# Kernel optimization log

Hardware: AMD Instinct MI355X
Metric: run time of the kernel (lower is better)

The kernel has to match this reference:

```python
import jax, jax.numpy as jnp
import numpy as np

N = 4_194_304  # number of sample points


def _make_C():
    # Faithful reproduction of the module's compliance matrix (including the
    # asymmetry: Ci[2,0]=Ci[2,1]=-vp, NOT -vp/Ep, exactly as in the source).
    vp, Ep = 0.4, 0.21
    Ci = np.zeros((6, 6), dtype=np.float64)
    Ci[0, 0] = 1 / Ep;  Ci[0, 1] = -vp / Ep; Ci[0, 2] = -vp / Ep
    Ci[1, 0] = -vp / Ep; Ci[1, 1] = 1 / Ep;  Ci[1, 2] = -vp / Ep
    Ci[2, 0] = -vp;      Ci[2, 1] = -vp;     Ci[2, 2] = 1 / Ep
    Ci[3, 3] = 2 * (1 + vp) / Ep
    Ci[4, 4] = 2 * (1 + vp) / Ep
    Ci[5, 5] = 2 * (1 + vp) / Ep
    return jnp.asarray(np.linalg.inv(Ci), dtype=jnp.float32)

_C = _make_C()  # [6, 6] stiffness matrix


def setup_inputs() -> dict:
    key = jax.random.key(0)
    k1, k2, k3, k4 = jax.random.split(key, 4)
    return {
        "grad_u": jax.random.normal(k1, (N, 3), dtype=jnp.float32),
        "grad_v": jax.random.normal(k2, (N, 3), dtype=jnp.float32),
        "grad_w": jax.random.normal(k3, (N, 3), dtype=jnp.float32),
        "gt_sdf": jax.random.normal(k4, (N,), dtype=jnp.float32),
    }


def reference(grad_u, grad_v, grad_w, gt_sdf):
    # Build per-point strain tensor in Voigt-like notation: [N, 6]
    et = jnp.stack([
        grad_u[:, 0],
        grad_v[:, 1],
        grad_w[:, 2],
        (grad_u[:, 1] + grad_v[:, 0]) * 0.5,
        (grad_u[:, 2] + grad_w[:, 0]) * 0.5,
        (grad_w[:, 1] + grad_v[:, 2]) * 0.5,
    ], axis=1)
    # Per-point quadratic form et_i^T C et_i == diag(et @ C @ et.T) without the
    # O(N^2) intermediate the torch code materializes.
    q = jnp.einsum('ni,ij,nj->n', et, _C, et)
    # Mask = points with gt_sdf < 1e-8 (index_select in torch; masked here so
    # shapes stay static under jit). Excluded points contribute 0 to the norm.
    mask = gt_sdf < 1e-8
    qm = jnp.where(mask, q, 0.0)
    count = jnp.sum(mask).astype(et.dtype)  # et.shape[0] after index_select
    W = jnp.sqrt(jnp.sum(qm * qm))           # L2 norm of the diagonal vector
    return W / count
```

## Files before the change

### kernel.cpp

```cpp
#include <hip/hip_runtime.h>
#include <math.h>

struct CParams {
    float b[3][3];
    float s;
};

static CParams make_C() {
    const double vp = 0.4, Ep = 0.21;
    double A[3][3] = {
        {1.0 / Ep, -vp / Ep, -vp / Ep},
        {-vp / Ep, 1.0 / Ep, -vp / Ep},
        {-vp,      -vp,      1.0 / Ep},
    };
    double inv[3][3] = {{1, 0, 0}, {0, 1, 0}, {0, 0, 1}};
    for (int col = 0; col < 3; ++col) {
        int piv = col;
        for (int r = col + 1; r < 3; ++r)
            if (fabs(A[r][col]) > fabs(A[piv][col])) piv = r;
        if (piv != col) {
            for (int c = 0; c < 3; ++c) {
                double t = A[col][c]; A[col][c] = A[piv][c]; A[piv][c] = t;
                t = inv[col][c]; inv[col][c] = inv[piv][c]; inv[piv][c] = t;
            }
        }
        double d = A[col][col];
        for (int c = 0; c < 3; ++c) { A[col][c] /= d; inv[col][c] /= d; }
        for (int r = 0; r < 3; ++r) {
            if (r == col) continue;
            double f = A[r][col];
            for (int c = 0; c < 3; ++c) {
                A[r][c] -= f * A[col][c];
                inv[r][c] -= f * inv[col][c];
            }
        }
    }
    CParams p;
    for (int i = 0; i < 3; ++i)
        for (int j = 0; j < 3; ++j)
            p.b[i][j] = (float)inv[i][j];
    p.s = (float)(Ep / (2.0 * (1.0 + vp)));
    return p;
}

static const CParams g_C = make_C();

#define MAXB 2048
#define TPB  256
#define TILE 256
#define F4A  192

#define ZERO4 make_float4(0.0f, 0.0f, 0.0f, 0.0f)

__global__ __launch_bounds__(TPB) void biomech_reduce(
    const float* __restrict__ gu, const float* __restrict__ gv,
    const float* __restrict__ gw, const float* __restrict__ gs,
    float* __restrict__ ws, int n, CParams C)
{
    __shared__ float4 buf[TPB / 64][3][F4A];

    const int wave    = threadIdx.x >> 6;
    const int lane    = threadIdx.x & 63;
    const int nwaves  = gridDim.x * (TPB / 64);
    const int ngroups = n / TILE;

    const float4* u4 = (const float4*)gu;
    const float4* v4 = (const float4*)gv;
    const float4* w4 = (const float4*)gw;

    float sumq2 = 0.0f, cnt = 0.0f;

    float4 pu0 = ZERO4, pu1 = ZERO4, pu2 = ZERO4;
    float4 pv0 = ZERO4, pv1 = ZERO4, pv2 = ZERO4;
    float4 pw0 = ZERO4, pw1 = ZERO4, pw2 = ZERO4;
    float  ps0 = 1.0f, ps1 = 1.0f, ps2 = 1.0f, ps3 = 1.0f;

    {
        const int g = blockIdx.x * (TPB / 64) + wave;
        if (g < ngroups) {
            const int b  = g * F4A;
            const int sb = g * TILE;
            pu0 = u4[b + lane]; pu1 = u4[b + 64 + lane]; pu2 = u4[b + 128 + lane];
            pv0 = v4[b + lane]; pv1 = v4[b + 64 + lane]; pv2 = v4[b + 128 + lane];
            pw0 = w4[b + lane]; pw1 = w4[b + 64 + lane]; pw2 = w4[b + 128 + lane];
            ps0 = gs[sb + lane];       ps1 = gs[sb + 64 + lane];
            ps2 = gs[sb + 128 + lane]; ps3 = gs[sb + 192 + lane];
        }
    }

    for (int gb = blockIdx.x * (TPB / 64); gb < ngroups; gb += nwaves) {
        const int g  = gb + wave;
        const int gn = g + nwaves;

        float4 nu0 = ZERO4, nu1 = ZERO4, nu2 = ZERO4;
        float4 nv0 = ZERO4, nv1 = ZERO4, nv2 = ZERO4;
        float4 nw0 = ZERO4, nw1 = ZERO4, nw2 = ZERO4;
        float  ns0 = 1.0f, ns1 = 1.0f, ns2 = 1.0f, ns3 = 1.0f;
        if (gn < ngroups) {
            const int b  = gn * F4A;
            const int sb = gn * TILE;
            nu0 = u4[b + lane]; nu1 = u4[b + 64 + lane]; nu2 = u4[b + 128 + lane];
            nv0 = v4[b + lane]; nv1 = v4[b + 64 + lane]; nv2 = v4[b + 128 + lane];
            nw0 = w4[b + lane]; nw1 = w4[b + 64 + lane]; nw2 = w4[b + 128 + lane];
            ns0 = gs[sb + lane];       ns1 = gs[sb + 64 + lane];
            ns2 = gs[sb + 128 + lane]; ns3 = gs[sb + 192 + lane];
        }

        if (g < ngroups) {
            buf[wave][0][lane] = pu0; buf[wave][0][64 + lane] = pu1; buf[wave][0][128 + lane] = pu2;
            buf[wave][1][lane] = pv0; buf[wave][1][64 + lane] = pv1; buf[wave][1][128 + lane] = pv2;
            buf[wave][2][lane] = pw0; buf[wave][2][64 + lane] = pw1; buf[wave][2][128 + lane] = pw2;
        }

        __syncthreads();

        if (g < ngroups) {
            const float* bu = (const float*)&buf[wave][0][0];
            const float* bv = (const float*)&buf[wave][1][0];
            const float* bw = (const float*)&buf[wave][2][0];
            const float sd[4] = {ps0, ps1, ps2, ps3};

#pragma unroll
            for (int k = 0; k < 4; ++k) {
                const int p = lane + (k << 6);
                float u0 = bu[3 * p], u1 = bu[3 * p + 1], u2 = bu[3 * p + 2];
                float v0 = bv[3 * p], v1 = bv[3 * p + 1], v2 = bv[3 * p + 2];
                float w0 = bw[3 * p], w1 = bw[3 * p + 1], w2 = bw[3 * p + 2];

                float e0 = u0, e1 = v1, e2 = w2;
                float e3 = 0.5f * (u1 + v0);
                float e4 = 0.5f * (u2 + w0);
                float e5 = 0.5f * (w1 + v2);

                float q = e0 * (C.b[0][0] * e0 + C.b[0][1] * e1 + C.b[0][2] * e2)
                        + e1 * (C.b[1][0] * e0 + C.b[1][1] * e1 + C.b[1][2] * e2)
                        + e2 * (C.b[2][0] * e0 + C.b[2][1] * e1 + C.b[2][2] * e2)
                        + C.s * (e3 * e3 + e4 * e4 + e5 * e5);

                bool m = sd[k] < 1e-8f;
                float qm = m ? q : 0.0f;
                sumq2 += qm * qm;
                cnt   += m ? 1.0f : 0.0f;
            }
        }

        __syncthreads();

        pu0 = nu0; pu1 = nu1; pu2 = nu2;
        pv0 = nv0; pv1 = nv1; pv2 = nv2;
        pw0 = nw0; pw1 = nw1; pw2 = nw2;
        ps0 = ns0; ps1 = ns1; ps2 = ns2; ps3 = ns3;
    }

    if (blockIdx.x == 0 && threadIdx.x == 0) {
        for (int i = (n / TILE) * TILE; i < n; ++i) {
            float e0 = gu[3 * i + 0];
            float e1 = gv[3 * i + 1];
            float e2 = gw[3 * i + 2];
            float e3 = 0.5f * (gu[3 * i + 1] + gv[3 * i + 0]);
            float e4 = 0.5f * (gu[3 * i + 2] + gw[3 * i + 0]);
            float e5 = 0.5f * (gw[3 * i + 1] + gv[3 * i + 2]);
            float q = e0 * (C.b[0][0] * e0 + C.b[0][1] * e1 + C.b[0][2] * e2)
                    + e1 * (C.b[1][0] * e0 + C.b[1][1] * e1 + C.b[1][2] * e2)
                    + e2 * (C.b[2][0] * e0 + C.b[2][1] * e1 + C.b[2][2] * e2)
                    + C.s * (e3 * e3 + e4 * e4 + e5 * e5);
            bool m = gs[i] < 1e-8f;
            float qm = m ? q : 0.0f;
            sumq2 += qm * qm;
            cnt   += m ? 1.0f : 0.0f;
        }
    }

#pragma unroll
    for (int off = 32; off > 0; off >>= 1) {
        sumq2 += __shfl_down(sumq2, off);
        cnt   += __shfl_down(cnt, off);
    }

    __shared__ float ssum[4], scnt[4];
    if (lane == 0) { ssum[wave] = sumq2; scnt[wave] = cnt; }
    __syncthreads();
    if (threadIdx.x == 0) {
        float s2 = 0.0f, c2 = 0.0f;
#pragma unroll
        for (int i = 0; i < 4; ++i) { s2 += ssum[i]; c2 += scnt[i]; }
        ws[blockIdx.x]        = s2;
        ws[MAXB + blockIdx.x] = c2;
    }
}

__global__ __launch_bounds__(256) void biomech_finalize(
    const float* __restrict__ ws, float* __restrict__ out, int nb)
{
    float s = 0.0f, c = 0.0f;
    for (int i = threadIdx.x; i < nb; i += 256) {
        s += ws[i];
        c += ws[MAXB + i];
    }
#pragma unroll
    for (int off = 32; off > 0; off >>= 1) {
        s += __shfl_down(s, off);
        c += __shfl_down(c, off);
    }
    __shared__ float ssum[4], scnt[4];
    const int wave = threadIdx.x >> 6;
    const int lane = threadIdx.x & 63;
    if (lane == 0) { ssum[wave] = s; scnt[wave] = c; }
    __syncthreads();
    if (threadIdx.x == 0) {
        float s2 = ssum[0] + ssum[1] + ssum[2] + ssum[3];
        float c2 = scnt[0] + scnt[1] + scnt[2] + scnt[3];
        out[0] = sqrtf(s2) / c2;
    }
}

extern "C" void kernel_launch(void* const* d_in, const int* in_sizes, int n_in,
                              void* d_out, int out_size, void* d_ws, size_t ws_size,
                              hipStream_t stream) {
    const float* gu = (const float*)d_in[0];
    const float* gv = (const float*)d_in[1];
    const float* gw = (const float*)d_in[2];
    const float* gs = (const float*)d_in[3];
    float* ws = (float*)d_ws;
    float* out = (float*)d_out;

    const int n = in_sizes[3];
    const int ngroups = n / TILE;
    const int wpb = TPB / 64;

    int grid = (ngroups + wpb - 1) / wpb;
    if (grid > 1024) grid = 1024;
    if (grid > MAXB) grid = MAXB;
    while (grid > 1 && (size_t)(MAXB + grid) * sizeof(float) > ws_size) grid >>= 1;
    if (grid < 1) grid = 1;

    biomech_reduce<<<grid, TPB, 0, stream>>>(gu, gv, gw, gs, ws, n, g_C);
    biomech_finalize<<<1, 256, 0, stream>>>(ws, out, grid);
}
```

Measured before the change: 179.3 us.

## Replace LDS-staged transpose with per-thread 4-point float4 loads

Removes the shared-memory staging buffer, the software prefetch and the two block barriers per iteration. Each thread now loads three consecutive float4s per gradient array plus one float4 of sdf, covering four points, and unpacks them in registers. The grid cap also rises from 1024 to 2048 blocks. Global loads become strided per lane (each lane reads 48 contiguous bytes), which may coalesce less well than the previous lane-contiguous pattern, in exchange for no LDS traffic and no synchronisation.

```diff
diff --git a/kernel.cpp b/kernel.cpp
--- a/kernel.cpp
+++ b/kernel.cpp
@@ -47,127 +47,68 @@
 
 #define MAXB 2048
 #define TPB  256
-#define TILE 256
-#define F4A  192
 
-#define ZERO4 make_float4(0.0f, 0.0f, 0.0f, 0.0f)
+__device__ __forceinline__ void accum_point(
+    float u0, float u1, float u2,
+    float v0, float v1, float v2,
+    float w0, float w1, float w2,
+    float sd, const CParams& C, float& sumq2, float& cnt)
+{
+    float e0 = u0, e1 = v1, e2 = w2;
+    float e3 = 0.5f * (u1 + v0);
+    float e4 = 0.5f * (u2 + w0);
+    float e5 = 0.5f * (w1 + v2);
+
+    float q = e0 * (C.b[0][0] * e0 + C.b[0][1] * e1 + C.b[0][2] * e2)
+            + e1 * (C.b[1][0] * e0 + C.b[1][1] * e1 + C.b[1][2] * e2)
+            + e2 * (C.b[2][0] * e0 + C.b[2][1] * e1 + C.b[2][2] * e2)
+            + C.s * (e3 * e3 + e4 * e4 + e5 * e5);
+
+    bool m = sd < 1e-8f;
+    float qm = m ? q : 0.0f;
+    sumq2 += qm * qm;
+    cnt   += m ? 1.0f : 0.0f;
+}
 
 __global__ __launch_bounds__(TPB) void biomech_reduce(
     const float* __restrict__ gu, const float* __restrict__ gv,
     const float* __restrict__ gw, const float* __restrict__ gs,
     float* __restrict__ ws, int n, CParams C)
 {
-    __shared__ float4 buf[TPB / 64][3][F4A];
-
-    const int wave    = threadIdx.x >> 6;
-    const int lane    = threadIdx.x & 63;
-    const int nwaves  = gridDim.x * (TPB / 64);
-    const int ngroups = n / TILE;
+    const int tid    = blockIdx.x * TPB + threadIdx.x;
+    const int stride = gridDim.x * TPB;
+    const int nvec   = n >> 2;
 
     const float4* u4 = (const float4*)gu;
     const float4* v4 = (const float4*)gv;
     const float4* w4 = (const float4*)gw;
+    const float4* s4 = (const float4*)gs;
 
     float sumq2 = 0.0f, cnt = 0.0f;
 
-    float4 pu0 = ZERO4, pu1 = ZERO4, pu2 = ZERO4;
-    float4 pv0 = ZERO4, pv1 = ZERO4, pv2 = ZERO4;
-    float4 pw0 = ZERO4, pw1 = ZERO4, pw2 = ZERO4;
-    float  ps0 = 1.0f, ps1 = 1.0f, ps2 = 1.0f, ps3 = 1.0f;
+    for (int i = tid; i < nvec; i += stride) {
+        const int b = 3 * i;
+        float4 a0 = u4[b], a1 = u4[b + 1], a2 = u4[b + 2];
+        float4 b0 = v4[b], b1 = v4[b + 1], b2 = v4[b + 2];
+        float4 c0 = w4[b], c1 = w4[b + 1], c2 = w4[b + 2];
+        float4 sd = s4[i];
 
-    {
-        const int g = blockIdx.x * (TPB / 64) + wave;
-        if (g < ngroups) {
-            const int b  = g * F4A;
-            const int sb = g * TILE;
-            pu0 = u4[b + lane]; pu1 = u4[b + 64 + lane]; pu2 = u4[b + 128 + lane];
-            pv0 = v4[b + lane]; pv1 = v4[b + 64 + lane]; pv2 = v4[b + 128 + lane];
-            pw0 = w4[b + lane]; pw1 = w4[b + 64 + lane]; pw2 = w4[b + 128 + lane];
-            ps0 = gs[sb + lane];       ps1 = gs[sb + 64 + lane];
-            ps2 = gs[sb + 128 + lane]; ps3 = gs[sb + 192 + lane];
-        }
-    }
-
-    for (int gb = blockIdx.x * (TPB / 64); gb < ngroups; gb += nwaves) {
-        const int g  = gb + wave;
-        const int gn = g + nwaves;
-
-        float4 nu0 = ZERO4, nu1 = ZERO4, nu2 = ZERO4;
-        float4 nv0 = ZERO4, nv1 = ZERO4, nv2 = ZERO4;
-        float4 nw0 = ZERO4, nw1 = ZERO4, nw2 = ZERO4;
-        float  ns0 = 1.0f, ns1 = 1.0f, ns2 = 1.0f, ns3 = 1.0f;
-        if (gn < ngroups) {
-            const int b  = gn * F4A;
-            const int sb = gn * TILE;
-            nu0 = u4[b + lane]; nu1 = u4[b + 64 + lane]; nu2 = u4[b + 128 + lane];
-            nv0 = v4[b + lane]; nv1 = v4[b + 64 + lane]; nv2 = v4[b + 128 + lane];
-            nw0 = w4[b + lane]; nw1 = w4[b + 64 + lane]; nw2 = w4[b + 128 + lane];
-            ns0 = gs[sb + lane];       ns1 = gs[sb + 64 + lane];
-            ns2 = gs[sb + 128 + lane]; ns3 = gs[sb + 192 + lane];
-        }
-
-        if (g < ngroups) {
-            buf[wave][0][lane] = pu0; buf[wave][0][64 + lane] = pu1; buf[wave][0][128 + lane] = pu2;
-            buf[wave][1][lane] = pv0; buf[wave][1][64 + lane] = pv1; buf[wave][1][128 + lane] = pv2;
-            buf[wave][2][lane] = pw0; buf[wave][2][64 + lane] = pw1; buf[wave][2][128 + lane] = pw2;
-        }
-
-        __syncthreads();
-
-        if (g < ngroups) {
-            const float* bu = (const float*)&buf[wave][0][0];
-            const float* bv = (const float*)&buf[wave][1][0];
-            const float* bw = (const float*)&buf[wave][2][0];
-            const float sd[4] = {ps0, ps1, ps2, ps3};
-
-#pragma unroll
-            for (int k = 0; k < 4; ++k) {
-                const int p = lane + (k << 6);
-                float u0 = bu[3 * p], u1 = bu[3 * p + 1], u2 = bu[3 * p + 2];
-                float v0 = bv[3 * p], v1 = bv[3 * p + 1], v2 = bv[3 * p + 2];
-                float w0 = bw[3 * p], w1 = bw[3 * p + 1], w2 = bw[3 * p + 2];
-
-                float e0 = u0, e1 = v1, e2 = w2;
-                float e3 = 0.5f * (u1 + v0);
-                float e4 = 0.5f * (u2 + w0);
-                float e5 = 0.5f * (w1 + v2);
-
-                float q = e0 * (C.b[0][0] * e0 + C.b[0][1] * e1 + C.b[0][2] * e2)
-                        + e1 * (C.b[1][0] * e0 + C.b[1][1] * e1 + C.b[1][2] * e2)
-                        + e2 * (C.b[2][0] * e0 + C.b[2][1] * e1 + C.b[2][2] * e2)
-                        + C.s * (e3 * e3 + e4 * e4 + e5 * e5);
-
-                bool m = sd[k] < 1e-8f;
-                float qm = m ? q : 0.0f;
-                sumq2 += qm * qm;
-                cnt   += m ? 1.0f : 0.0f;
-            }
-        }
-
-        __syncthreads();
-
-        pu0 = nu0; pu1 = nu1; pu2 = nu2;
-        pv0 = nv0; pv1 = nv1; pv2 = nv2;
-        pw0 = nw0; pw1 = nw1; pw2 = nw2;
-        ps0 = ns0; ps1 = ns1; ps2 = ns2; ps3 = ns3;
+        accum_point(a0.x, a0.y, a0.z,  b0.x, b0.y, b0.z,  c0.x, c0.y, c0.z,
+                    sd.x, C, sumq2, cnt);
+        accum_point(a0.w, a1.x, a1.y,  b0.w, b1.x, b1.y,  c0.w, c1.x, c1.y,
+                    sd.y, C, sumq2, cnt);
+        accum_point(a1.z, a1.w, a2.x,  b1.z, b1.w, b2.x,  c1.z, c1.w, c2.x,
+                    sd.z, C, sumq2, cnt);
+        accum_point(a2.y, a2.z, a2.w,  b2.y, b2.z, b2.w,  c2.y, c2.z, c2.w,
+                    sd.w, C, sumq2, cnt);
     }
 
     if (blockIdx.x == 0 && threadIdx.x == 0) {
-        for (int i = (n / TILE) * TILE; i < n; ++i) {
-            float e0 = gu[3 * i + 0];
-            float e1 = gv[3 * i + 1];
-            float e2 = gw[3 * i + 2];
-            float e3 = 0.5f * (gu[3 * i + 1] + gv[3 * i + 0]);
-            float e4 = 0.5f * (gu[3 * i + 2] + gw[3 * i + 0]);
-            float e5 = 0.5f * (gw[3 * i + 1] + gv[3 * i + 2]);
-            float q = e0 * (C.b[0][0] * e0 + C.b[0][1] * e1 + C.b[0][2] * e2)
-                    + e1 * (C.b[1][0] * e0 + C.b[1][1] * e1 + C.b[1][2] * e2)
-                    + e2 * (C.b[2][0] * e0 + C.b[2][1] * e1 + C.b[2][2] * e2)
-                    + C.s * (e3 * e3 + e4 * e4 + e5 * e5);
-            bool m = gs[i] < 1e-8f;
-            float qm = m ? q : 0.0f;
-            sumq2 += qm * qm;
-            cnt   += m ? 1.0f : 0.0f;
+        for (int i = nvec * 4; i < n; ++i) {
+            accum_point(gu[3 * i], gu[3 * i + 1], gu[3 * i + 2],
+                        gv[3 * i], gv[3 * i + 1], gv[3 * i + 2],
+                        gw[3 * i], gw[3 * i + 1], gw[3 * i + 2],
+                        gs[i], C, sumq2, cnt);
         }
     }
 
@@ -177,13 +118,15 @@
         cnt   += __shfl_down(cnt, off);
     }
 
-    __shared__ float ssum[4], scnt[4];
+    __shared__ float ssum[TPB / 64], scnt[TPB / 64];
+    const int wave = threadIdx.x >> 6;
+    const int lane = threadIdx.x & 63;
     if (lane == 0) { ssum[wave] = sumq2; scnt[wave] = cnt; }
     __syncthreads();
     if (threadIdx.x == 0) {
         float s2 = 0.0f, c2 = 0.0f;
 #pragma unroll
-        for (int i = 0; i < 4; ++i) { s2 += ssum[i]; c2 += scnt[i]; }
+        for (int i = 0; i < TPB / 64; ++i) { s2 += ssum[i]; c2 += scnt[i]; }
         ws[blockIdx.x]        = s2;
         ws[MAXB + blockIdx.x] = c2;
     }
@@ -225,11 +168,10 @@
     float* out = (float*)d_out;
 
     const int n = in_sizes[3];
-    const int ngroups = n / TILE;
-    const int wpb = TPB / 64;
+    const int nvec = n >> 2;
 
-    int grid = (ngroups + wpb - 1) / wpb;
-    if (grid > 1024) grid = 1024;
+    int grid = (nvec + TPB - 1) / TPB;
+    if (grid > 2048) grid = 2048;
     if (grid > MAXB) grid = MAXB;
     while (grid > 1 && (size_t)(MAXB + grid) * sizeof(float) > ws_size) grid >>= 1;
     if (grid < 1) grid = 1;
```

Result: no change. 178.3 us (-0.6%).
